# Performance work log

Measured on AMD Instinct MI355X. Metric: run time of the kernel, lower is better.

## Reference

```python
import jax, jax.numpy as jnp
import numpy as np

B, H, W, C = 4, 128, 128, 512
HID, HEADS, BS = 768, 8, 8
NBH, NBW = H // BS, W // BS
NBT, BS2 = NBH * NBW, BS * BS
HD = HID // HEADS


def setup_inputs() -> dict:
    key = jax.random.key(0)
    k = jax.random.split(key, 5)
    x = jax.random.normal(k[0], (B, H, W, C), jnp.float32)
    # attn weights must sum to 1 over the last dim
    attn_weights = jax.nn.softmax(
        jax.random.normal(k[1], (HEADS, B, NBT, BS2, BS2), jnp.float32), axis=-1)
    reordered_indexes = jnp.arange(H * W, dtype=jnp.int32).reshape(1, H * W, 1)
    W_in = jax.random.normal(k[2], (C, 3 * HID), jnp.float32) * (C ** -0.5)
    b_in = jnp.zeros((3 * HID,), jnp.float32)
    W_out = jax.random.normal(k[3], (HID, C), jnp.float32) * 0.05 * (HID ** -0.5)
    b_out = jnp.zeros((C,), jnp.float32)
    return dict(x=x, attn_weights=attn_weights, W_in=W_in, b_in=b_in,
                W_out=W_out, b_out=b_out, reordered_indexes=reordered_indexes)


def reference(x, attn_weights, W_in, b_in, W_out, b_out, reordered_indexes):
    idx = reordered_indexes.reshape(-1)  # (H*W,) permutation shared across batch
    # gather / token reorder
    x = x.reshape(B, H * W, C)[:, idx, :].reshape(B, H, W, C)
    # in_proj + split into (s, v, y); Balancer/Whiten/Identity are identity in fwd
    p = x @ W_in + b_in  # (B,H,W,3*HID)
    s, v, y = jnp.split(p, 3, axis=-1)
    v = v * jnp.tanh(s)
    # to per-block head layout: (heads, B, num_block_tot, bs^2, head_dim)
    v = v.reshape(B, NBH, BS, NBW, BS, HEADS, HD)
    v = v.transpose(5, 0, 1, 3, 2, 4, 6).reshape(HEADS, B, NBT, BS2, HD)
    v = jnp.einsum('hbnij,hbnjd->hbnid', attn_weights, v)
    # back to (B,H,W,HID)
    v = v.reshape(HEADS, B, NBH, NBW, BS, BS, HD)
    v = v.transpose(1, 2, 4, 3, 5, 0, 6).reshape(B, H, W, HID)
    out = (v * y) @ W_out + b_out  # (B,H,W,C)
    # scatter back to original token order
    out = out.reshape(B, H * W, C)
    out = jnp.zeros_like(out).at[:, idx, :].set(out)
    return out.reshape(B, H, W, C)
```

## Files before the change

kernel.cpp:

```cpp
#include <hip/hip_runtime.h>
#include <cstdint>
#include <cstddef>

#define Bb     4
#define Cc     512
#define HID    768
#define HEADS  8
#define NBT    256
#define BS2    64
#define HD     96
#define HWTOK  16384
#define MTOK   65536
#define N3     2304

typedef __attribute__((ext_vector_type(8))) short frag16;
typedef __attribute__((ext_vector_type(4))) float f32x4;

__device__ __forceinline__ float b2f(unsigned short u) {
    union { unsigned int i; float f; } x; x.i = ((unsigned int)u) << 16; return x.f;
}
__device__ __forceinline__ unsigned short f2b(float f) {
    union { float f; unsigned int i; } x; x.f = f;
    unsigned int r = x.i + 0x7fffu + ((x.i >> 16) & 1u);
    return (unsigned short)(r >> 16);
}
union cvt8 { uint4 u; unsigned short s[8]; };

__device__ __forceinline__ void gl2lds16(const void* g, void* l) {
    __builtin_amdgcn_global_load_lds(
        (const __attribute__((address_space(1))) unsigned int*)g,
        (__attribute__((address_space(3))) unsigned int*)l, 16, 0, 0);
}

__device__ __forceinline__ float fast_tanh(float x) {
    float a = __builtin_fabsf(x);
    float t = __expf(-2.0f * a);
    float r = (1.0f - t) / (1.0f + t);
    return __builtin_copysignf(r, x);
}

__global__ __launch_bounds__(256) void k_transpose(
    const float* __restrict__ w, unsigned short* __restrict__ wt,
    int K, int N) {
    int e = blockIdx.x * 256 + threadIdx.x;
    if (e < K * N) {
        int k = e / N, n = e - k * N;
        wt[(size_t)n * K + k] = f2b(w[e]);
    }
}

__global__ __launch_bounds__(256) void k_gather(
    const float* __restrict__ x, const int* __restrict__ idx,
    unsigned short* __restrict__ xg) {
    int gid = blockIdx.x * 256 + threadIdx.x;
    int t = gid >> 6, col = (gid & 63) * 8;
    int bb = t >> 14, hw = t & 16383;
    const float* src = x + ((size_t)bb * HWTOK + idx[hw]) * Cc + col;
    float4 f0 = *(const float4*)src, f1 = *(const float4*)(src + 4);
    cvt8 c;
    c.s[0] = f2b(f0.x); c.s[1] = f2b(f0.y); c.s[2] = f2b(f0.z); c.s[3] = f2b(f0.w);
    c.s[4] = f2b(f1.x); c.s[5] = f2b(f1.y); c.s[6] = f2b(f1.z); c.s[7] = f2b(f1.w);
    *(uint4*)(xg + (size_t)t * Cc + col) = c.u;
}

__global__ __launch_bounds__(256) void k_inproj(
    const unsigned short* __restrict__ xg,
    const unsigned short* __restrict__ winT,
    const float* __restrict__ b_in,
    unsigned short* __restrict__ y_img,
    unsigned short* __restrict__ vt_blk) {
    __shared__ alignas(16) unsigned short smem[2][4096 + 6144];
    const int tid = threadIdx.x;
    const int wv = tid >> 6, lane = tid & 63;
    const int wm = wv >> 1, wn = wv & 1;
    const int fr = lane & 15, q = lane >> 4;
    const int n0 = blockIdx.x * 64;
    const int m0 = blockIdx.y * 128;

    const unsigned short* gsrc[5];
    int loff[5];
    #pragma unroll
    for (int ci = 0; ci < 5; ci++) {
        int c = wv * 5 + ci;
        if (c < 8) {
            gsrc[ci] = xg + (size_t)(m0 + c * 16 + fr) * Cc + q * 8;
            loff[ci] = c * 512;
        } else {
            int cb = c - 8, sl = cb >> 2;
            gsrc[ci] = winT + (size_t)(sl * HID + n0 + (cb & 3) * 16 + fr) * Cc + q * 8;
            loff[ci] = 4096 + cb * 512;
        }
    }

    f32x4 acc[3][2][4];
    #pragma unroll
    for (int sl = 0; sl < 3; sl++)
        #pragma unroll
        for (int nt = 0; nt < 2; nt++)
            #pragma unroll
            for (int mt = 0; mt < 4; mt++) acc[sl][nt][mt] = (f32x4){0.f,0.f,0.f,0.f};

    #pragma unroll
    for (int ci = 0; ci < 5; ci++)
        gl2lds16(gsrc[ci], &smem[0][loff[ci]]);
    __syncthreads();

    #pragma unroll 2
    for (int kt = 1; kt <= 16; kt++) {
        if (kt < 16) {
            #pragma unroll
            for (int ci = 0; ci < 5; ci++)
                gl2lds16(gsrc[ci] + kt * 32, &smem[kt & 1][loff[ci]]);
        }
        const unsigned short* sa = smem[(kt - 1) & 1];
        frag16 af[4];
        #pragma unroll
        for (int mt = 0; mt < 4; mt++)
            af[mt] = *(const frag16*)(sa + (wm * 4 + mt) * 512 + lane * 8);
        #pragma unroll
        for (int sl = 0; sl < 3; sl++) {
            #pragma unroll
            for (int nt = 0; nt < 2; nt++) {
                frag16 bf = *(const frag16*)(sa + 4096 +
                                             (sl * 4 + wn * 2 + nt) * 512 + lane * 8);
                #pragma unroll
                for (int mt = 0; mt < 4; mt++)
                    acc[sl][nt][mt] = __builtin_amdgcn_mfma_f32_16x16x32_bf16(
                        af[mt], bf, acc[sl][nt][mt], 0, 0, 0);
            }
        }
        __syncthreads();
    }

    #pragma unroll
    for (int nt = 0; nt < 2; nt++) {
        const int j = n0 + wn * 32 + nt * 16 + fr;
        const float bs = b_in[j], bv = b_in[HID + j], by = b_in[2 * HID + j];
        const int h = j / HD, d = j - h * HD;
        #pragma unroll
        for (int mt = 0; mt < 4; mt++) {
            #pragma unroll
            for (int r = 0; r < 4; r++) {
                const int t = m0 + wm * 64 + mt * 16 + q * 4 + r;
                const int bb = t >> 14, hw = t & 16383;
                const float sv = acc[0][nt][mt][r] + bs;
                const float vv = acc[1][nt][mt][r] + bv;
                const float yv = acc[2][nt][mt][r] + by;
                y_img[(size_t)t * HID + j] = f2b(yv);
                const int hr = hw >> 7, wc = hw & 127;
                const int nblk = ((hr >> 3) << 4) | (wc >> 3);
                const int ii   = ((hr & 7) << 3) | (wc & 7);
                vt_blk[((((size_t)h * Bb + bb) * NBT + nblk) * BS2 + ii) * HD + d] =
                    f2b(vv * fast_tanh(sv));
            }
        }
    }
}

__global__ __launch_bounds__(256) void k_attn(
    const float* __restrict__ attnw,
    const unsigned short* __restrict__ vt_blk,
    unsigned short* __restrict__ y_img) {
    __shared__ alignas(16) unsigned short Aat[64][72];
    __shared__ alignas(16) unsigned short VtT[96][72];
    const int tid = threadIdx.x;
    const int g = blockIdx.x;
    const int wv = tid >> 6, lane = tid & 63;
    const int fr = lane & 15, q = lane >> 4;
    const int wm = wv >> 1, wn = wv & 1;

    const float* asrc = attnw + (size_t)g * 4096;
    const unsigned short* vsrc = vt_blk + (size_t)g * 6144;
    #pragma unroll
    for (int r = 0; r < 2; r++) {
        int v = tid + 256 * r;
        int i = v >> 3, jj = (v & 7) * 8;
        const float* ap = asrc + (size_t)v * 8;
        float4 f0 = *(const float4*)ap, f1 = *(const float4*)(ap + 4);
        cvt8 c;
        c.s[0]=f2b(f0.x); c.s[1]=f2b(f0.y); c.s[2]=f2b(f0.z); c.s[3]=f2b(f0.w);
        c.s[4]=f2b(f1.x); c.s[5]=f2b(f1.y); c.s[6]=f2b(f1.z); c.s[7]=f2b(f1.w);
        *(uint4*)(&Aat[i][jj]) = c.u;
    }
    #pragma unroll
    for (int r = 0; r < 3; r++) {
        int v = tid + 256 * r;
        int j = v / 12, dq = v - j * 12;
        cvt8 c; c.u = ((const uint4*)vsrc)[v];
        #pragma unroll
        for (int e = 0; e < 8; e++) VtT[dq * 8 + e][j] = c.s[e];
    }
    __syncthreads();

    f32x4 acc[2][3];
    #pragma unroll
    for (int mt = 0; mt < 2; mt++)
        #pragma unroll
        for (int nd = 0; nd < 3; nd++) acc[mt][nd] = (f32x4){0.f,0.f,0.f,0.f};
    #pragma unroll
    for (int kk = 0; kk < 2; kk++) {
        frag16 af[2];
        #pragma unroll
        for (int mt = 0; mt < 2; mt++)
            af[mt] = *(const frag16*)(&Aat[wm * 32 + mt * 16 + fr][kk * 32 + q * 8]);
        #pragma unroll
        for (int nd = 0; nd < 3; nd++) {
            frag16 bf = *(const frag16*)(&VtT[wn * 48 + nd * 16 + fr][kk * 32 + q * 8]);
            #pragma unroll
            for (int mt = 0; mt < 2; mt++)
                acc[mt][nd] = __builtin_amdgcn_mfma_f32_16x16x32_bf16(
                    af[mt], bf, acc[mt][nd], 0, 0, 0);
        }
    }

    const int h = g >> 10, b = (g >> 8) & 3, n = g & 255;
    #pragma unroll
    for (int nd = 0; nd < 3; nd++) {
        const int d = wn * 48 + nd * 16 + fr;
        #pragma unroll
        for (int mt = 0; mt < 2; mt++) {
            #pragma unroll
            for (int r = 0; r < 4; r++) {
                const int i = wm * 32 + mt * 16 + q * 4 + r;
                const int hr = ((n >> 4) << 3) | (i >> 3);
                const int wc = ((n & 15) << 3) | (i & 7);
                const size_t t = ((size_t)b << 14) + (size_t)hr * 128 + wc;
                const size_t off = t * HID + (size_t)h * HD + d;
                y_img[off] = f2b(acc[mt][nd][r] * b2f(y_img[off]));
            }
        }
    }
}

__global__ __launch_bounds__(256) void k_outproj(
    const unsigned short* __restrict__ avy,
    const unsigned short* __restrict__ woutT,
    const float* __restrict__ b_out,
    const int* __restrict__ idx,
    float* __restrict__ out) {
    __shared__ alignas(16) unsigned short smem[2][8192];
    const int tid = threadIdx.x;
    const int wv = tid >> 6, lane = tid & 63;
    const int wm = wv >> 1, wn = wv & 1;
    const int fr = lane & 15, q = lane >> 4;
    const int c0 = blockIdx.x * 128;
    const int m0 = blockIdx.y * 128;

    const unsigned short* gsrc[4];
    int loff[4];
    #pragma unroll
    for (int ci = 0; ci < 4; ci++) {
        int c = wv * 4 + ci;
        if (c < 8) {
            gsrc[ci] = avy + (size_t)(m0 + c * 16 + fr) * HID + q * 8;
            loff[ci] = c * 512;
        } else {
            int cb = c - 8;
            gsrc[ci] = woutT + (size_t)(c0 + cb * 16 + fr) * HID + q * 8;
            loff[ci] = 4096 + cb * 512;
        }
    }

    f32x4 acc[4][4];
    #pragma unroll
    for (int nt = 0; nt < 4; nt++)
        #pragma unroll
        for (int mt = 0; mt < 4; mt++) acc[nt][mt] = (f32x4){0.f,0.f,0.f,0.f};

    #pragma unroll
    for (int ci = 0; ci < 4; ci++)
        gl2lds16(gsrc[ci], &smem[0][loff[ci]]);
    __syncthreads();

    #pragma unroll 2
    for (int kt = 1; kt <= 24; kt++) {
        if (kt < 24) {
            #pragma unroll
            for (int ci = 0; ci < 4; ci++)
                gl2lds16(gsrc[ci] + kt * 32, &smem[kt & 1][loff[ci]]);
        }
        const unsigned short* sa = smem[(kt - 1) & 1];
        frag16 af[4];
        #pragma unroll
        for (int mt = 0; mt < 4; mt++)
            af[mt] = *(const frag16*)(sa + (wm * 4 + mt) * 512 + lane * 8);
        #pragma unroll
        for (int nt = 0; nt < 4; nt++) {
            frag16 bf = *(const frag16*)(sa + 4096 + (wn * 4 + nt) * 512 + lane * 8);
            #pragma unroll
            for (int mt = 0; mt < 4; mt++)
                acc[nt][mt] = __builtin_amdgcn_mfma_f32_16x16x32_bf16(
                    af[mt], bf, acc[nt][mt], 0, 0, 0);
        }
        __syncthreads();
    }

    #pragma unroll
    for (int nt = 0; nt < 4; nt++) {
        const int c = c0 + wn * 64 + nt * 16 + fr;
        const float bo = b_out[c];
        #pragma unroll
        for (int mt = 0; mt < 4; mt++) {
            #pragma unroll
            for (int r = 0; r < 4; r++) {
                const int t = m0 + wm * 64 + mt * 16 + q * 4 + r;
                const int bb = t >> 14, hw = t & 16383;
                const int dst = idx[hw];
                out[((size_t)bb * HWTOK + dst) * Cc + c] = acc[nt][mt][r] + bo;
            }
        }
    }
}

extern "C" void kernel_launch(void* const* d_in, const int* in_sizes, int n_in,
                              void* d_out, int out_size, void* d_ws, size_t ws_size,
                              hipStream_t stream) {
    const float* x     = (const float*)d_in[0];
    const float* attnw = (const float*)d_in[1];
    const float* W_in  = (const float*)d_in[2];
    const float* b_in  = (const float*)d_in[3];
    const float* W_out = (const float*)d_in[4];
    const float* b_out = (const float*)d_in[5];
    const int*   idx   = (const int*)d_in[6];
    float*       out   = (float*)d_out;

    char* p = (char*)d_ws;
    unsigned short* winT  = (unsigned short*)p; p += (size_t)N3 * Cc * 2;
    unsigned short* woutT = (unsigned short*)p; p += (size_t)Cc * HID * 2;
    unsigned short* vt    = (unsigned short*)p; p += (size_t)HEADS * Bb * NBT * BS2 * HD * 2;
    unsigned short* y_img = (unsigned short*)p; p += (size_t)MTOK * HID * 2;
    unsigned short* xg = (unsigned short*)d_out;

    k_transpose<<<(N3 * Cc + 255) / 256, 256, 0, stream>>>(W_in, winT, Cc, N3);
    k_transpose<<<(HID * Cc + 255) / 256, 256, 0, stream>>>(W_out, woutT, HID, Cc);
    k_gather<<<MTOK * 64 / 256, 256, 0, stream>>>(x, idx, xg);

    dim3 g1(HID / 64, MTOK / 128);
    k_inproj<<<g1, 256, 0, stream>>>(xg, winT, b_in, y_img, vt);

    k_attn<<<HEADS * Bb * NBT, 256, 0, stream>>>(attnw, vt, y_img);

    dim3 g3(Cc / 128, MTOK / 128);
    k_outproj<<<g3, 256, 0, stream>>>(y_img, woutT, b_out, idx, out);
}
```

Baseline: 773.4 us.

## Deepen GEMM pipelines to four LDS stages with XCD-aware block swizzle

Both the in-projection and out-projection GEMMs move from double buffering to a four-slot LDS ring with two tiles in flight. They replace __syncthreads with explicit vmcnt waits plus one s_barrier per step, and raise wave priority around the MFMA block. Block indices are also remapped so consecutive blocks on the same XCD (fb&7) share M/N tiles for better L2 reuse. The intent is to hide global-to-LDS latency and cut barrier count. The cost is more LDS per block, which may reduce occupancy, and the hand-written vmcnt counts must match the number of loads issued per step.

New measurement: 754.4 us. 1.03x faster.

```diff
diff --git a/kernel.cpp b/kernel.cpp
--- a/kernel.cpp
+++ b/kernel.cpp
@@ -69,13 +69,16 @@
     const float* __restrict__ b_in,
     unsigned short* __restrict__ y_img,
     unsigned short* __restrict__ vt_blk) {
-    __shared__ alignas(16) unsigned short smem[2][4096 + 6144];
+    __shared__ alignas(16) unsigned short smem[4][10240];
     const int tid = threadIdx.x;
     const int wv = tid >> 6, lane = tid & 63;
     const int wm = wv >> 1, wn = wv & 1;
     const int fr = lane & 15, q = lane >> 4;
-    const int n0 = blockIdx.x * 64;
-    const int m0 = blockIdx.y * 128;
+
+    const int fb = blockIdx.x + 12 * blockIdx.y;
+    const int sb = (fb & 7) * 768 + (fb >> 3);
+    const int n0 = (sb % 12) * 64;
+    const int m0 = (sb / 12) * 128;
 
     const unsigned short* gsrc[5];
     int loff[5];
@@ -101,22 +104,30 @@
             for (int mt = 0; mt < 4; mt++) acc[sl][nt][mt] = (f32x4){0.f,0.f,0.f,0.f};
 
     #pragma unroll
-    for (int ci = 0; ci < 5; ci++)
-        gl2lds16(gsrc[ci], &smem[0][loff[ci]]);
-    __syncthreads();
-
-    #pragma unroll 2
-    for (int kt = 1; kt <= 16; kt++) {
-        if (kt < 16) {
+    for (int ci = 0; ci < 5; ci++) gl2lds16(gsrc[ci], &smem[0][loff[ci]]);
+    #pragma unroll
+    for (int ci = 0; ci < 5; ci++) gl2lds16(gsrc[ci] + 32, &smem[1][loff[ci]]);
+
+    #pragma unroll
+    for (int t = 0; t < 16; t++) {
+        if (t < 14) {
+            const int bi = (t + 2) & 3;
             #pragma unroll
             for (int ci = 0; ci < 5; ci++)
-                gl2lds16(gsrc[ci] + kt * 32, &smem[kt & 1][loff[ci]]);
-        }
-        const unsigned short* sa = smem[(kt - 1) & 1];
+                gl2lds16(gsrc[ci] + (t + 2) * 32, &smem[bi][loff[ci]]);
+            asm volatile("s_waitcnt vmcnt(10)" ::: "memory");
+        } else if (t == 14) {
+            asm volatile("s_waitcnt vmcnt(5)" ::: "memory");
+        } else {
+            asm volatile("s_waitcnt vmcnt(0)" ::: "memory");
+        }
+        __builtin_amdgcn_s_barrier();
+        const unsigned short* sa = smem[t & 3];
         frag16 af[4];
         #pragma unroll
         for (int mt = 0; mt < 4; mt++)
             af[mt] = *(const frag16*)(sa + (wm * 4 + mt) * 512 + lane * 8);
+        __builtin_amdgcn_s_setprio(1);
         #pragma unroll
         for (int sl = 0; sl < 3; sl++) {
             #pragma unroll
@@ -129,7 +140,7 @@
                         af[mt], bf, acc[sl][nt][mt], 0, 0, 0);
             }
         }
-        __syncthreads();
+        __builtin_amdgcn_s_setprio(0);
     }
 
     #pragma unroll
@@ -238,13 +249,16 @@
     const float* __restrict__ b_out,
     const int* __restrict__ idx,
     float* __restrict__ out) {
-    __shared__ alignas(16) unsigned short smem[2][8192];
+    __shared__ alignas(16) unsigned short smem[4][8192];
     const int tid = threadIdx.x;
     const int wv = tid >> 6, lane = tid & 63;
     const int wm = wv >> 1, wn = wv & 1;
     const int fr = lane & 15, q = lane >> 4;
-    const int c0 = blockIdx.x * 128;
-    const int m0 = blockIdx.y * 128;
+
+    const int fb = blockIdx.x + 4 * blockIdx.y;
+    const int sb = (fb & 7) * 256 + (fb >> 3);
+    const int c0 = (sb % 4) * 128;
+    const int m0 = (sb / 4) * 128;
 
     const unsigned short* gsrc[4];
     int loff[4];
@@ -268,22 +282,30 @@
         for (int mt = 0; mt < 4; mt++) acc[nt][mt] = (f32x4){0.f,0.f,0.f,0.f};
 
     #pragma unroll
-    for (int ci = 0; ci < 4; ci++)
-        gl2lds16(gsrc[ci], &smem[0][loff[ci]]);
-    __syncthreads();
-
-    #pragma unroll 2
-    for (int kt = 1; kt <= 24; kt++) {
-        if (kt < 24) {
+    for (int ci = 0; ci < 4; ci++) gl2lds16(gsrc[ci], &smem[0][loff[ci]]);
+    #pragma unroll
+    for (int ci = 0; ci < 4; ci++) gl2lds16(gsrc[ci] + 32, &smem[1][loff[ci]]);
+
+    #pragma unroll
+    for (int t = 0; t < 24; t++) {
+        if (t < 22) {
+            const int bi = (t + 2) & 3;
             #pragma unroll
             for (int ci = 0; ci < 4; ci++)
-                gl2lds16(gsrc[ci] + kt * 32, &smem[kt & 1][loff[ci]]);
-        }
-        const unsigned short* sa = smem[(kt - 1) & 1];
+                gl2lds16(gsrc[ci] + (t + 2) * 32, &smem[bi][loff[ci]]);
+            asm volatile("s_waitcnt vmcnt(8)" ::: "memory");
+        } else if (t == 22) {
+            asm volatile("s_waitcnt vmcnt(4)" ::: "memory");
+        } else {
+            asm volatile("s_waitcnt vmcnt(0)" ::: "memory");
+        }
+        __builtin_amdgcn_s_barrier();
+        const unsigned short* sa = smem[t & 3];
         frag16 af[4];
         #pragma unroll
         for (int mt = 0; mt < 4; mt++)
             af[mt] = *(const frag16*)(sa + (wm * 4 + mt) * 512 + lane * 8);
+        __builtin_amdgcn_s_setprio(1);
         #pragma unroll
         for (int nt = 0; nt < 4; nt++) {
             frag16 bf = *(const frag16*)(sa + 4096 + (wn * 4 + nt) * 512 + lane * 8);
@@ -292,7 +314,7 @@
                 acc[nt][mt] = __builtin_amdgcn_mfma_f32_16x16x32_bf16(
                     af[mt], bf, acc[nt][mt], 0, 0, 0);
         }
-        __syncthreads();
+        __builtin_amdgcn_s_setprio(0);
     }
 
     #pragma unroll
```
